# Kernel tuning notes

Measured on AMD Instinct MI355X. Metric: run time of the kernel, lower is better.

Reference implementation:

```python
import jax, jax.numpy as jnp
import numpy as np

B, D, G, K, NP = 8, 1024, 32, 64, 1024


def setup_inputs() -> dict:
    key = jax.random.key(0)
    ks = jax.random.split(key, 7)
    x = jax.random.normal(ks[0], (B, NP, D), jnp.float32)
    weights = jax.random.uniform(ks[1], (B, G), jnp.float32)
    xopt = jax.random.normal(ks[2], (B, D), jnp.float32)
    R = jax.random.normal(ks[3], (K, K), jnp.float32) / np.sqrt(K).astype(np.float32)
    group_indices = jax.random.randint(ks[4], (B, G, K), 0, D)
    valid_mask = jax.random.randint(ks[5], (B, G, K), 0, 2).astype(bool)
    group_counts = jax.random.randint(ks[6], (B,), 1, G + 1)
    return dict(x=x, weights=weights, xopt=xopt, R=R,
                group_indices=group_indices, valid_mask=valid_mask,
                group_counts=group_counts)


def reference(x, weights, xopt, R, group_indices, valid_mask, group_counts):
    Bb, NPp, Dd = x.shape
    Gg, Kk = group_indices.shape[1], group_indices.shape[2]
    # elliptic coefficients 1e6**linspace(0,1,K), a deterministic buffer
    coeffs = jnp.asarray(1.0e6, x.dtype) ** jnp.linspace(0.0, 1.0, Kk).astype(x.dtype)
    z = x - xopt[:, None, :]                                   # (B,NP,D)
    # gather per-group sub-vectors without materializing (B,G,NP,D):
    # zb: (NP,D), ib: (G,K) -> zb[:, ib]: (NP,G,K)
    z_sub = jax.vmap(lambda zb, ib: zb[:, ib])(z, group_indices)  # (B,NP,G,K)
    z_sub = jnp.transpose(z_sub, (0, 2, 1, 3))                 # (B,G,NP,K)
    # per-group small rotation
    z_rot = jnp.einsum('bgnk,kl->bgnl', z_sub, R)              # (B,G,NP,K)
    # mask invalid dims of each group, elliptic weighted sum over K
    masked_coeffs = jnp.where(valid_mask[:, :, None, :], coeffs[None, None, None, :],
                              jnp.zeros((), x.dtype))          # (B,G,NP->bcast,K)
    elliptic_vals = jnp.sum(masked_coeffs * z_rot * z_rot, axis=-1)  # (B,G,NP)
    # mask invalid groups, weighted reduce over groups
    group_valid = (jnp.arange(Gg)[None, :] < group_counts[:, None]).astype(x.dtype)  # (B,G)
    fitness = jnp.einsum('bgn,bg->bn', elliptic_vals, weights * group_valid)  # (B,NP)
    return fitness
```

## Files before the change

kernel.cpp:

```cpp
#include <hip/hip_runtime.h>
#include <hip/hip_fp16.h>

#define B_     8
#define D_     1024
#define G_     32
#define K_     64
#define NP_    1024
#define ROWS   32
#define TPB    1024
#define STRIDE 1026

__global__ __launch_bounds__(TPB, 4) void fitness(
    const float* __restrict__ x,
    const float* __restrict__ weights,
    const float* __restrict__ xopt,
    const float* __restrict__ R,
    const int* __restrict__ gidx,
    const int* __restrict__ mask,
    const int* __restrict__ counts,
    float* __restrict__ out) {
  __shared__ __half zh[ROWS * STRIDE];
  __shared__ int    gli[G_ * K_];
  __shared__ float  ctab[K_];
  __shared__ float  red[16][64];

  const int tile = blockIdx.x;
  const int b    = blockIdx.y;
  const int t    = threadIdx.x;

  if (t < K_) ctab[t] = exp2f((float)t * (19.931568569324174f / 63.0f));

  gli[t]       = gidx[b * (G_ * K_) + t];
  gli[t + TPB] = gidx[b * (G_ * K_) + TPB + t];

  {
    const float4* x4  = (const float4*)(x + ((size_t)(b * NP_ + tile * ROWS)) * D_);
    const float4* xo4 = (const float4*)(xopt + b * D_);
    const int col4 = t & 255;
    float4 xo = xo4[col4];
#pragma unroll
    for (int j = 0; j < (ROWS * 256) / TPB; ++j) {
      int chunk = t + TPB * j;
      int row = chunk >> 8;
      float4 xv = x4[row * 256 + col4];
      __half2* p = (__half2*)(zh + row * STRIDE + col4 * 4);
      p[0] = __floats2half2_rn(xv.x - xo.x, xv.y - xo.y);
      p[1] = __floats2half2_rn(xv.z - xo.z, xv.w - xo.w);
    }
  }
  __syncthreads();

  const int wv   = t >> 6;
  const int lane = t & 63;
  const int row  = lane & 31;
  const int h    = lane >> 5;
  const int cnt  = counts[b];

  float fit = 0.0f;

  if (2 * wv < cnt) {
    const int g  = 2 * wv + h;
    const int bg = b * G_ + g;
    const __half* myrow = zh + row * STRIDE;
    const int*    gb    = gli + g * K_;

    float S[K_];
#pragma unroll
    for (int l = 0; l < K_; ++l) S[l] = 0.0f;

    for (int k = 0; k < K_; ++k) {
      int   gk = gb[k];
      float zk = __half2float(myrow[gk]);
      const float* rk = R + k * K_;
#pragma unroll
      for (int l = 0; l < K_; ++l) S[l] = fmaf(zk, rk[l], S[l]);
    }

    float wm = (g < cnt) ? weights[bg] : 0.0f;
    const int4* m4 = (const int4*)(mask + bg * K_);
#pragma unroll
    for (int q = 0; q < K_ / 4; ++q) {
      int4 mm = m4[q];
      float c0 = ctab[4 * q + 0], c1 = ctab[4 * q + 1];
      float c2 = ctab[4 * q + 2], c3 = ctab[4 * q + 3];
      float s0 = S[4 * q + 0], s1 = S[4 * q + 1];
      float s2 = S[4 * q + 2], s3 = S[4 * q + 3];
      fit = fmaf(mm.x ? wm * c0 : 0.0f, s0 * s0, fit);
      fit = fmaf(mm.y ? wm * c1 : 0.0f, s1 * s1, fit);
      fit = fmaf(mm.z ? wm * c2 : 0.0f, s2 * s2, fit);
      fit = fmaf(mm.w ? wm * c3 : 0.0f, s3 * s3, fit);
    }
  }

  red[wv][lane] = fit;
  __syncthreads();

  if (t < ROWS) {
    float s = 0.0f;
#pragma unroll
    for (int w2 = 0; w2 < 16; ++w2) s += red[w2][t] + red[w2][t + 32];
    out[b * NP_ + tile * ROWS + t] = s;
  }
}

extern "C" void kernel_launch(void* const* d_in, const int* in_sizes, int n_in,
                              void* d_out, int out_size, void* d_ws, size_t ws_size,
                              hipStream_t stream) {
  const float* x       = (const float*)d_in[0];
  const float* weights = (const float*)d_in[1];
  const float* xopt    = (const float*)d_in[2];
  const float* R       = (const float*)d_in[3];
  const int*   gidx    = (const int*)d_in[4];
  const int*   mask    = (const int*)d_in[5];
  const int*   counts  = (const int*)d_in[6];
  float*       out     = (float*)d_out;

  fitness<<<dim3(NP_ / ROWS, B_), dim3(TPB), 0, stream>>>(
      x, weights, xopt, R, gidx, mask, counts, out);
}
```

Before: 107.5 us.

## Compute per-group rotation with MFMA f16 matrix instructions instead of scalar FMAs

```diff
diff --git a/kernel.cpp b/kernel.cpp
--- a/kernel.cpp
+++ b/kernel.cpp
@@ -1,5 +1,8 @@
 #include <hip/hip_runtime.h>
-#include <hip/hip_fp16.h>
+
+typedef _Float16 half8  __attribute__((ext_vector_type(8)));
+typedef _Float16 half4h __attribute__((ext_vector_type(4)));
+typedef float    f32x4  __attribute__((ext_vector_type(4)));
 
 #define B_     8
 #define D_     1024
@@ -8,9 +11,9 @@
 #define NP_    1024
 #define ROWS   32
 #define TPB    1024
-#define STRIDE 1026
+#define STRIDE 1028
 
-__global__ __launch_bounds__(TPB, 4) void fitness(
+__global__ __launch_bounds__(TPB) void fitness(
     const float* __restrict__ x,
     const float* __restrict__ weights,
     const float* __restrict__ xopt,
@@ -19,19 +22,47 @@
     const int* __restrict__ mask,
     const int* __restrict__ counts,
     float* __restrict__ out) {
-  __shared__ __half zh[ROWS * STRIDE];
-  __shared__ int    gli[G_ * K_];
-  __shared__ float  ctab[K_];
-  __shared__ float  red[16][64];
+  __shared__ _Float16 zh[ROWS * STRIDE];
+  __shared__ int      gli[G_ * K_];
+  __shared__ _Float16 Rb[8 * 512];
+  __shared__ float    wcs[G_ * K_];
+  __shared__ float    redrow[ROWS];
 
   const int tile = blockIdx.x;
   const int b    = blockIdx.y;
   const int t    = threadIdx.x;
+  const int cnt  = counts[b];
 
-  if (t < K_) ctab[t] = exp2f((float)t * (19.931568569324174f / 63.0f));
+  gli[t]        = gidx[b * (G_ * K_) + t];
+  gli[t + 1024] = gidx[b * (G_ * K_) + 1024 + t];
 
-  gli[t]       = gidx[b * (G_ * K_) + t];
-  gli[t + TPB] = gidx[b * (G_ * K_) + TPB + t];
+  {
+    const float C = 19.931568569324174f / 63.0f;
+#pragma unroll
+    for (int r = 0; r < 2; ++r) {
+      int idx = t + r * 1024;
+      int g = idx >> 6, l = idx & 63;
+      bool v = (g < cnt) && (mask[b * (G_ * K_) + idx] != 0);
+      wcs[idx] = v ? weights[b * G_ + g] * exp2f((float)l * C) : 0.0f;
+    }
+  }
+
+  {
+    int pos  = t * 4;
+    int frag = pos >> 9, rem = pos & 511;
+    int lane = rem >> 3, j0 = rem & 7;
+    int kt = frag >> 2, nt = frag & 3;
+    int quad = lane >> 4, ln = lane & 15;
+    half4h rv;
+#pragma unroll
+    for (int e = 0; e < 4; ++e) {
+      int k = kt * 32 + quad * 8 + j0 + e;
+      rv[e] = (_Float16)R[k * K_ + nt * 16 + ln];
+    }
+    *(half4h*)(Rb + pos) = rv;
+  }
+
+  if (t < ROWS) redrow[t] = 0.0f;
 
   {
     const float4* x4  = (const float4*)(x + ((size_t)(b * NP_ + tile * ROWS)) * D_);
@@ -40,67 +71,78 @@
     float4 xo = xo4[col4];
 #pragma unroll
     for (int j = 0; j < (ROWS * 256) / TPB; ++j) {
-      int chunk = t + TPB * j;
-      int row = chunk >> 8;
+      int row = (t >> 8) + 4 * j;
       float4 xv = x4[row * 256 + col4];
-      __half2* p = (__half2*)(zh + row * STRIDE + col4 * 4);
-      p[0] = __floats2half2_rn(xv.x - xo.x, xv.y - xo.y);
-      p[1] = __floats2half2_rn(xv.z - xo.z, xv.w - xo.w);
+      half4h hv;
+      hv[0] = (_Float16)(xv.x - xo.x);
+      hv[1] = (_Float16)(xv.y - xo.y);
+      hv[2] = (_Float16)(xv.z - xo.z);
+      hv[3] = (_Float16)(xv.w - xo.w);
+      *(half4h*)(zh + row * STRIDE + col4 * 4) = hv;
     }
   }
   __syncthreads();
 
   const int wv   = t >> 6;
   const int lane = t & 63;
-  const int row  = lane & 31;
-  const int h    = lane >> 5;
-  const int cnt  = counts[b];
+  const int quad = lane >> 4;
+  const int ln   = lane & 15;
+  const int items = 2 * cnt;
 
-  float fit = 0.0f;
+  const half8* rbf = (const half8*)Rb;
 
-  if (2 * wv < cnt) {
-    const int g  = 2 * wv + h;
-    const int bg = b * G_ + g;
-    const __half* myrow = zh + row * STRIDE;
-    const int*    gb    = gli + g * K_;
+  for (int i = wv; i < items; i += 16) {
+    const int g     = i >> 1;
+    const int mtile = i & 1;
 
-    float S[K_];
+    const int* gp = gli + g * K_ + quad * 8;
+    int4 i0 = *(const int4*)(gp);
+    int4 i1 = *(const int4*)(gp + 4);
+    int4 i2 = *(const int4*)(gp + 32);
+    int4 i3 = *(const int4*)(gp + 36);
+    const _Float16* zr = zh + (mtile * 16 + ln) * STRIDE;
+    half8 a0, a1;
+    a0[0] = zr[i0.x]; a0[1] = zr[i0.y]; a0[2] = zr[i0.z]; a0[3] = zr[i0.w];
+    a0[4] = zr[i1.x]; a0[5] = zr[i1.y]; a0[6] = zr[i1.z]; a0[7] = zr[i1.w];
+    a1[0] = zr[i2.x]; a1[1] = zr[i2.y]; a1[2] = zr[i2.z]; a1[3] = zr[i2.w];
+    a1[4] = zr[i3.x]; a1[5] = zr[i3.y]; a1[6] = zr[i3.z]; a1[7] = zr[i3.w];
+
+    f32x4 c0 = {0.f, 0.f, 0.f, 0.f}, c1 = c0, c2 = c0, c3 = c0;
+    c0 = __builtin_amdgcn_mfma_f32_16x16x32_f16(a0, rbf[0 * 64 + lane], c0, 0, 0, 0);
+    c1 = __builtin_amdgcn_mfma_f32_16x16x32_f16(a0, rbf[1 * 64 + lane], c1, 0, 0, 0);
+    c2 = __builtin_amdgcn_mfma_f32_16x16x32_f16(a0, rbf[2 * 64 + lane], c2, 0, 0, 0);
+    c3 = __builtin_amdgcn_mfma_f32_16x16x32_f16(a0, rbf[3 * 64 + lane], c3, 0, 0, 0);
+    c0 = __builtin_amdgcn_mfma_f32_16x16x32_f16(a1, rbf[4 * 64 + lane], c0, 0, 0, 0);
+    c1 = __builtin_amdgcn_mfma_f32_16x16x32_f16(a1, rbf[5 * 64 + lane], c1, 0, 0, 0);
+    c2 = __builtin_amdgcn_mfma_f32_16x16x32_f16(a1, rbf[6 * 64 + lane], c2, 0, 0, 0);
+    c3 = __builtin_amdgcn_mfma_f32_16x16x32_f16(a1, rbf[7 * 64 + lane], c3, 0, 0, 0);
+
+    const float* wg = wcs + g * K_ + ln;
+    float w0 = wg[0], w1 = wg[16], w2 = wg[32], w3 = wg[48];
+    float q0, q1, q2, q3;
+    q0 = w0 * c0[0] * c0[0] + w1 * c1[0] * c1[0] + w2 * c2[0] * c2[0] + w3 * c3[0] * c3[0];
+    q1 = w0 * c0[1] * c0[1] + w1 * c1[1] * c1[1] + w2 * c2[1] * c2[1] + w3 * c3[1] * c3[1];
+    q2 = w0 * c0[2] * c0[2] + w1 * c1[2] * c1[2] + w2 * c2[2] * c2[2] + w3 * c3[2] * c3[2];
+    q3 = w0 * c0[3] * c0[3] + w1 * c1[3] * c1[3] + w2 * c2[3] * c2[3] + w3 * c3[3] * c3[3];
+
 #pragma unroll
-    for (int l = 0; l < K_; ++l) S[l] = 0.0f;
-
-    for (int k = 0; k < K_; ++k) {
-      int   gk = gb[k];
-      float zk = __half2float(myrow[gk]);
-      const float* rk = R + k * K_;
-#pragma unroll
-      for (int l = 0; l < K_; ++l) S[l] = fmaf(zk, rk[l], S[l]);
+    for (int off = 1; off < 16; off <<= 1) {
+      q0 += __shfl_xor(q0, off);
+      q1 += __shfl_xor(q1, off);
+      q2 += __shfl_xor(q2, off);
+      q3 += __shfl_xor(q3, off);
     }
-
-    float wm = (g < cnt) ? weights[bg] : 0.0f;
-    const int4* m4 = (const int4*)(mask + bg * K_);
-#pragma unroll
-    for (int q = 0; q < K_ / 4; ++q) {
-      int4 mm = m4[q];
-      float c0 = ctab[4 * q + 0], c1 = ctab[4 * q + 1];
-      float c2 = ctab[4 * q + 2], c3 = ctab[4 * q + 3];
-      float s0 = S[4 * q + 0], s1 = S[4 * q + 1];
-      float s2 = S[4 * q + 2], s3 = S[4 * q + 3];
-      fit = fmaf(mm.x ? wm * c0 : 0.0f, s0 * s0, fit);
-      fit = fmaf(mm.y ? wm * c1 : 0.0f, s1 * s1, fit);
-      fit = fmaf(mm.z ? wm * c2 : 0.0f, s2 * s2, fit);
-      fit = fmaf(mm.w ? wm * c3 : 0.0f, s3 * s3, fit);
+    if (ln == 0) {
+      float* rr = redrow + mtile * 16 + quad * 4;
+      atomicAdd(rr + 0, q0);
+      atomicAdd(rr + 1, q1);
+      atomicAdd(rr + 2, q2);
+      atomicAdd(rr + 3, q3);
     }
   }
-
-  red[wv][lane] = fit;
   __syncthreads();
 
-  if (t < ROWS) {
-    float s = 0.0f;
-#pragma unroll
-    for (int w2 = 0; w2 < 16; ++w2) s += red[w2][t] + red[w2][t + 32];
-    out[b * NP_ + tile * ROWS + t] = s;
-  }
+  if (t < ROWS) out[b * NP_ + tile * ROWS + t] = redrow[t];
 }
 
 extern "C" void kernel_launch(void* const* d_in, const int* in_sizes, int n_in,
```

Measured after the change: 90.17 us. 16.1% less time.
